# Kernel tuning notes

Hardware: AMD Instinct MI355X
Metric: run time of the kernel (lower is better)

Reference implementation:

```python
import jax, jax.numpy as jnp
import numpy as np

EPS = 1e-6
QMAX = 127.0


def _smooth_quant_linear(x, w):
    """SmoothQuant int8 linear: out = dequant(quant(x/s) @ quant(w*s)^T).
    x: [T, D] activations, w: [O, D] weights. Returns [T, O] float32.
    """
    amax_x = jnp.max(jnp.abs(x), axis=0)          # [D] per-in-channel act max
    amax_w = jnp.max(jnp.abs(w), axis=0)          # [D] per-in-channel weight max
    # smooth scale s_j = sqrt(amax_x_j / amax_w_j)  (alpha = 0.5)
    s = jnp.sqrt(jnp.maximum(amax_x, EPS) / jnp.maximum(amax_w, EPS))
    s = jnp.maximum(s, EPS)
    xs = x / s                                    # smoothed activations
    ws = w * s                                    # smoothed weights
    x_scale = jnp.maximum(jnp.max(jnp.abs(xs), axis=-1, keepdims=True), EPS) / QMAX  # [T,1] per-token
    w_scale = jnp.maximum(jnp.max(jnp.abs(ws), axis=-1, keepdims=True), EPS) / QMAX  # [O,1] per-row
    x_q = jnp.clip(jnp.round(xs / x_scale), -QMAX, QMAX)   # int8-valued, kept f32 for GEMM
    w_q = jnp.clip(jnp.round(ws / w_scale), -QMAX, QMAX)
    # int8 GEMM + dequant with per-token / per-channel scales
    return (x_q @ w_q.T) * x_scale * w_scale.T


def _expert_forward(xe, guw, dw):
    # xe: [T, dim], guw: [2*ims, dim], dw: [dim, ims]
    h = _smooth_quant_linear(xe, guw)             # [T, 2*ims]
    gate, up = jnp.split(h, 2, axis=-1)           # [T, ims] each
    a = jax.nn.silu(gate) * up                    # SwiGLU
    return _smooth_quant_linear(a, dw)            # [T, dim]


def setup_inputs() -> dict:
    key = jax.random.key(0)
    k1, k2, k3 = jax.random.split(key, 3)
    E, T, D, I = 8, 2048, 2048, 1024
    x = jax.random.normal(k1, (E, T, D), dtype=jnp.float32)
    gate_up_weight = jax.random.normal(k2, (E, 2 * I, D), dtype=jnp.float32) * 0.02
    down_weight = jax.random.normal(k3, (E, D, I), dtype=jnp.float32) * 0.02
    return {"x": x, "gate_up_weight": gate_up_weight, "down_weight": down_weight}


def reference(x, gate_up_weight, down_weight):
    # Grouped per-expert SmoothQuant SwiGLU MLP: vmap over the expert axis.
    return jax.vmap(_expert_forward)(x, gate_up_weight, down_weight)
```

## Files before the change

kernel.cpp:

```cpp
#include <hip/hip_runtime.h>
#include <stdint.h>

constexpr int E_ = 8, T_ = 2048, D_ = 2048, I_ = 1024;
#define EPS_ 1e-6f
#define QMAX_ 127.0f

typedef int v4i __attribute__((ext_vector_type(4)));
typedef uint32_t __attribute__((address_space(1))) u32g_t;
typedef uint32_t __attribute__((address_space(3))) u32l_t;

__device__ __forceinline__ void load_lds16(const void* g, void* l) {
  __builtin_amdgcn_global_load_lds((u32g_t*)(uintptr_t)g, (u32l_t*)(uintptr_t)l,
                                   16, 0, 0);
}

template <int RPC>
__global__ __launch_bounds__(256) void colmax_partial(
    const float* __restrict__ src, float* __restrict__ partial, int cols) {
  int e = blockIdx.z, rc = blockIdx.y;
  int col = blockIdx.x * 256 + threadIdx.x;
  const float* p = src + ((size_t)e * gridDim.y + rc) * RPC * cols + col;
  float m = 0.f;
#pragma unroll 8
  for (int r = 0; r < RPC; ++r) m = fmaxf(m, fabsf(p[(size_t)r * cols]));
  partial[((size_t)e * gridDim.y + rc) * cols + col] = m;
}

__global__ __launch_bounds__(256) void compute_s(
    const float* __restrict__ px, const float* __restrict__ pw,
    float* __restrict__ s, int cols) {
  int e = blockIdx.y;
  int c = blockIdx.x * 256 + threadIdx.x;
  float ax = 0.f, aw = 0.f;
  for (int k = 0; k < 16; ++k) {
    ax = fmaxf(ax, px[((size_t)e * 16 + k) * cols + c]);
    aw = fmaxf(aw, pw[((size_t)e * 16 + k) * cols + c]);
  }
  float sv = sqrtf(fmaxf(ax, EPS_) / fmaxf(aw, EPS_));
  s[(size_t)e * cols + c] = fmaxf(sv, EPS_);
}

template <bool MUL, int COLS>
__global__ __launch_bounds__(256) void quant_rows(
    const float* __restrict__ src, const float* __restrict__ s,
    int8_t* __restrict__ q, float* __restrict__ rscale, int nrows) {
  constexpr int NP = COLS / 256;
  int e = blockIdx.y;
  int row = blockIdx.x * 4 + (threadIdx.x >> 6);
  int lane = threadIdx.x & 63;
  const float4* row4 = (const float4*)(src + ((size_t)e * nrows + row) * COLS);
  const float4* s4 = (const float4*)(s + (size_t)e * COLS);
  float4 vv[NP];
  float m = 0.f;
#pragma unroll
  for (int i = 0; i < NP; ++i) {
    int c = i * 64 + lane;
    float4 rv = row4[c], sv = s4[c];
    float4 v;
    v.x = MUL ? rv.x * sv.x : rv.x / sv.x;
    v.y = MUL ? rv.y * sv.y : rv.y / sv.y;
    v.z = MUL ? rv.z * sv.z : rv.z / sv.z;
    v.w = MUL ? rv.w * sv.w : rv.w / sv.w;
    vv[i] = v;
    m = fmaxf(m, fmaxf(fmaxf(fabsf(v.x), fabsf(v.y)), fmaxf(fabsf(v.z), fabsf(v.w))));
  }
#pragma unroll
  for (int off = 32; off > 0; off >>= 1) m = fmaxf(m, __shfl_xor(m, off, 64));
  float scale = fmaxf(m, EPS_) / QMAX_;
  char4* qrow = (char4*)(q + ((size_t)e * nrows + row) * COLS);
#pragma unroll
  for (int i = 0; i < NP; ++i) {
    int c = i * 64 + lane;
    float4 v = vv[i];
    char4 o;
    o.x = (int8_t)fminf(fmaxf(rintf(v.x / scale), -QMAX_), QMAX_);
    o.y = (int8_t)fminf(fmaxf(rintf(v.y / scale), -QMAX_), QMAX_);
    o.z = (int8_t)fminf(fmaxf(rintf(v.z / scale), -QMAX_), QMAX_);
    o.w = (int8_t)fminf(fmaxf(rintf(v.w / scale), -QMAX_), QMAX_);
    qrow[c] = o;
  }
  if (lane == 0) rscale[(size_t)e * nrows + row] = scale;
}

template <bool FUSE, int K, int NOUT>
__global__ __launch_bounds__(256) void gemm_i8(
    const int8_t* __restrict__ Aq, const int8_t* __restrict__ Bq,
    const float* __restrict__ asc, const float* __restrict__ bsc,
    float* __restrict__ outp, float* __restrict__ pmax) {
  constexpr int BK = 64;
  constexpr int NK = K / BK;
  constexpr int NCH = FUSE ? 16 : 12;
  constexpr int CPW = NCH / 4;
  constexpr int TOT = 8192 + (FUSE ? 8192 : 4096);
  __shared__ int8_t lds[2][TOT];

  const int e = blockIdx.z;
  const int n0 = blockIdx.x * 64, m0 = blockIdx.y * 128;
  const int8_t* Ae = Aq + (size_t)e * T_ * K;
  const int8_t* Be = Bq + (size_t)e * 2048 * K;
  const int tid = threadIdx.x;
  const int lane = tid & 63, wv = tid >> 6;
  const int l16 = lane & 15, quad = lane >> 4;
  const int wm = wv & 1, wn = wv >> 1;
  const int lrow = lane >> 2;
  const int scol = ((lane & 3) ^ ((lane >> 3) & 3)) << 4;
  const int swsel = ((quad ^ ((l16 >> 1) & 3)) << 4);

  const int8_t* gsrc[CPW];
  int loff[CPW];
#pragma unroll
  for (int i = 0; i < CPW; ++i) {
    int c = wv * CPW + i;
    if (c < 8) {
      gsrc[i] = Ae + (size_t)(m0 + c * 16 + lrow) * K + scol;
      loff[i] = c * 1024;
    } else {
      int cc = c - 8;
      int br = n0 + ((FUSE && cc >= 4) ? I_ : 0) + (cc & 3) * 16 + lrow;
      gsrc[i] = Be + (size_t)br * K + scol;
      loff[i] = 8192 + cc * 1024;
    }
  }

  v4i accg[4][2], accu[4][2];
#pragma unroll
  for (int mt = 0; mt < 4; ++mt)
#pragma unroll
    for (int nt = 0; nt < 2; ++nt) {
      accg[mt][nt] = (v4i){0, 0, 0, 0};
      accu[mt][nt] = (v4i){0, 0, 0, 0};
    }

#pragma unroll
  for (int i = 0; i < CPW; ++i) load_lds16(gsrc[i], &lds[0][loff[i]]);
  __syncthreads();

  int cur = 0;
  for (int ks = 0; ks < NK; ++ks) {
    if (ks + 1 < NK) {
#pragma unroll
      for (int i = 0; i < CPW; ++i)
        load_lds16(gsrc[i] + (size_t)(ks + 1) * BK, &lds[cur ^ 1][loff[i]]);
    }
    const int8_t* La = &lds[cur][0];
    const int8_t* Lb = &lds[cur][8192];
    v4i af[4];
#pragma unroll
    for (int mt = 0; mt < 4; ++mt)
      af[mt] = *(const v4i*)(La + (wm * 64 + mt * 16 + l16) * 64 + swsel);
    v4i bf0[2], bf1[2];
#pragma unroll
    for (int nt = 0; nt < 2; ++nt) {
      int br = wn * 32 + nt * 16 + l16;
      bf0[nt] = *(const v4i*)(Lb + br * 64 + swsel);
      if (FUSE) bf1[nt] = *(const v4i*)(Lb + 4096 + br * 64 + swsel);
    }
#pragma unroll
    for (int mt = 0; mt < 4; ++mt)
#pragma unroll
      for (int nt = 0; nt < 2; ++nt) {
        accg[mt][nt] = __builtin_amdgcn_mfma_i32_16x16x64_i8(
            af[mt], bf0[nt], accg[mt][nt], 0, 0, 0);
        if (FUSE)
          accu[mt][nt] = __builtin_amdgcn_mfma_i32_16x16x64_i8(
              af[mt], bf1[nt], accu[mt][nt], 0, 0, 0);
      }
    __syncthreads();
    cur ^= 1;
  }

  const float* ascE = asc + (size_t)e * T_;
  const float* bscE = bsc + (size_t)e * 2048;
  float cml[2] = {0.f, 0.f};
#pragma unroll
  for (int mt = 0; mt < 4; ++mt)
#pragma unroll
    for (int nt = 0; nt < 2; ++nt)
#pragma unroll
      for (int r2 = 0; r2 < 4; ++r2) {
        int grow = m0 + wm * 64 + mt * 16 + quad * 4 + r2;
        int gcol = n0 + wn * 32 + nt * 16 + l16;
        float as = ascE[grow];
        if (FUSE) {
          float g = (float)accg[mt][nt][r2] * as * bscE[gcol];
          float u = (float)accu[mt][nt][r2] * as * bscE[I_ + gcol];
          float sg = g / (1.0f + expf(-g));
          float av = sg * u;
          outp[(size_t)e * T_ * NOUT + (size_t)grow * NOUT + gcol] = av;
          cml[nt] = fmaxf(cml[nt], fabsf(av));
        } else {
          outp[(size_t)e * T_ * NOUT + (size_t)grow * NOUT + gcol] =
              (float)accg[mt][nt][r2] * as * bscE[gcol];
        }
      }

  if (FUSE) {
    float* cmax = (float*)&lds[0][0];
    if (tid < 64) cmax[tid] = 0.f;
    __syncthreads();
#pragma unroll
    for (int nt = 0; nt < 2; ++nt)
      atomicMax((int*)&cmax[wn * 32 + nt * 16 + l16], __float_as_int(cml[nt]));
    __syncthreads();
    if (tid < 64)
      pmax[((size_t)e * 16 + blockIdx.y) * NOUT + n0 + tid] = cmax[tid];
  }
}

extern "C" void kernel_launch(void* const* d_in, const int* in_sizes, int n_in,
                              void* d_out, int out_size, void* d_ws, size_t ws_size,
                              hipStream_t stream) {
  const float* x   = (const float*)d_in[0];
  const float* guw = (const float*)d_in[1];
  const float* dw  = (const float*)d_in[2];
  float* out = (float*)d_out;

  char* ws = (char*)d_ws;
  size_t off = 0;
  auto alloc = [&](size_t bytes) { char* p = ws + off; off += bytes; return p; };
  int8_t* xq   = (int8_t*)alloc((size_t)E_ * T_ * D_);
  int8_t* wq1  = (int8_t*)alloc((size_t)E_ * 2 * I_ * D_);
  int8_t* aq   = (int8_t*)alloc((size_t)E_ * T_ * I_);
  int8_t* dwq  = (int8_t*)alloc((size_t)E_ * D_ * I_);
  float*  a    = (float*)alloc((size_t)E_ * T_ * I_ * 4);
  float*  px   = (float*)alloc((size_t)E_ * 16 * D_ * 4);
  float*  pw   = (float*)alloc((size_t)E_ * 16 * D_ * 4);
  float*  pdw  = (float*)alloc((size_t)E_ * 16 * I_ * 4);
  float*  pa   = (float*)alloc((size_t)E_ * 16 * I_ * 4);
  float*  s1   = (float*)alloc((size_t)E_ * D_ * 4);
  float*  s2   = (float*)alloc((size_t)E_ * I_ * 4);
  float*  xsc  = (float*)alloc((size_t)E_ * T_ * 4);
  float*  wsc1 = (float*)alloc((size_t)E_ * 2 * I_ * 4);
  float*  asc  = (float*)alloc((size_t)E_ * T_ * 4);
  float*  dwsc = (float*)alloc((size_t)E_ * D_ * 4);

  dim3 b(256);
  colmax_partial<128><<<dim3(D_ / 256, 16, E_), b, 0, stream>>>(x, px, D_);
  colmax_partial<128><<<dim3(D_ / 256, 16, E_), b, 0, stream>>>(guw, pw, D_);
  colmax_partial<128><<<dim3(I_ / 256, 16, E_), b, 0, stream>>>(dw, pdw, I_);
  compute_s<<<dim3(D_ / 256, E_), b, 0, stream>>>(px, pw, s1, D_);
  quant_rows<false, D_><<<dim3(T_ / 4, E_), b, 0, stream>>>(x, s1, xq, xsc, T_);
  quant_rows<true, D_><<<dim3(2 * I_ / 4, E_), b, 0, stream>>>(guw, s1, wq1, wsc1, 2 * I_);
  gemm_i8<true, D_, I_><<<dim3(I_ / 64, T_ / 128, E_), b, 0, stream>>>(
      xq, wq1, xsc, wsc1, a, pa);
  compute_s<<<dim3(I_ / 256, E_), b, 0, stream>>>(pa, pdw, s2, I_);
  quant_rows<false, I_><<<dim3(T_ / 4, E_), b, 0, stream>>>(a, s2, aq, asc, T_);
  quant_rows<true, I_><<<dim3(D_ / 4, E_), b, 0, stream>>>(dw, s2, dwq, dwsc, D_);
  gemm_i8<false, I_, D_><<<dim3(D_ / 64, T_ / 128, E_), b, 0, stream>>>(
      aq, dwq, asc, dwsc, out, nullptr);
}
```

Baseline: 601.0 us.

## Deepen GEMM pipeline to 4-slot LDS ring, widen down-proj tile, merge small launches

The int8 GEMM moves from a double buffer to a 4-slot LDS ring that prefetches two K-steps ahead. It uses explicit vmcnt waits and raw barriers instead of __syncthreads, and raises wave priority around the MFMA block. The down-projection GEMM now uses a 128-wide N tile so each block does more work per A load. The column-max kernels for x and gate/up are merged into one launch, and each activation/weight quantisation pair is merged into one launch to cut launch overhead. The larger LDS footprint (64KB per block) may reduce occupancy, and the hardcoded vmcnt literals tie correctness to exactly 4 chunks per wave.

```diff
diff --git a/kernel.cpp b/kernel.cpp
--- a/kernel.cpp
+++ b/kernel.cpp
@@ -12,6 +12,23 @@
 __device__ __forceinline__ void load_lds16(const void* g, void* l) {
   __builtin_amdgcn_global_load_lds((u32g_t*)(uintptr_t)g, (u32l_t*)(uintptr_t)l,
                                    16, 0, 0);
+}
+
+__global__ __launch_bounds__(256) void colmax_xw(
+    const float* __restrict__ x, const float* __restrict__ guw,
+    float* __restrict__ px, float* __restrict__ pw) {
+  int e = blockIdx.z, rc = blockIdx.y;
+  const float* src;
+  float* dst;
+  int rcc;
+  if (rc < 16) { src = x;   dst = px; rcc = rc; }
+  else         { src = guw; dst = pw; rcc = rc - 16; }
+  int col = blockIdx.x * 256 + threadIdx.x;
+  const float* p = src + ((size_t)e * 16 + rcc) * 128 * 2048 + col;
+  float m = 0.f;
+#pragma unroll 8
+  for (int r = 0; r < 128; ++r) m = fmaxf(m, fabsf(p[(size_t)r * 2048]));
+  dst[((size_t)e * 16 + rcc) * 2048 + col] = m;
 }
 
 template <int RPC>
@@ -41,15 +58,10 @@
 }
 
 template <bool MUL, int COLS>
-__global__ __launch_bounds__(256) void quant_rows(
-    const float* __restrict__ src, const float* __restrict__ s,
-    int8_t* __restrict__ q, float* __restrict__ rscale, int nrows) {
+__device__ __forceinline__ void quant_row_body(
+    const float4* __restrict__ row4, const float4* __restrict__ s4,
+    char4* __restrict__ qrow, float* __restrict__ rsc, int lane) {
   constexpr int NP = COLS / 256;
-  int e = blockIdx.y;
-  int row = blockIdx.x * 4 + (threadIdx.x >> 6);
-  int lane = threadIdx.x & 63;
-  const float4* row4 = (const float4*)(src + ((size_t)e * nrows + row) * COLS);
-  const float4* s4 = (const float4*)(s + (size_t)e * COLS);
   float4 vv[NP];
   float m = 0.f;
 #pragma unroll
@@ -67,7 +79,6 @@
 #pragma unroll
   for (int off = 32; off > 0; off >>= 1) m = fmaxf(m, __shfl_xor(m, off, 64));
   float scale = fmaxf(m, EPS_) / QMAX_;
-  char4* qrow = (char4*)(q + ((size_t)e * nrows + row) * COLS);
 #pragma unroll
   for (int i = 0; i < NP; ++i) {
     int c = i * 64 + lane;
@@ -79,23 +90,50 @@
     o.w = (int8_t)fminf(fmaxf(rintf(v.w / scale), -QMAX_), QMAX_);
     qrow[c] = o;
   }
-  if (lane == 0) rscale[(size_t)e * nrows + row] = scale;
-}
-
-template <bool FUSE, int K, int NOUT>
+  if (lane == 0) *rsc = scale;
+}
+
+template <int COLS>
+__global__ __launch_bounds__(256) void quant_pair(
+    const float* __restrict__ srcA, const float* __restrict__ srcB,
+    const float* __restrict__ s, int8_t* __restrict__ qA,
+    int8_t* __restrict__ qB, float* __restrict__ rscA,
+    float* __restrict__ rscB, int nrowsA, int nrowsB) {
+  int e = blockIdx.y;
+  int nbA = nrowsA >> 2;
+  bool isB = (int)blockIdx.x >= nbA;
+  int rb = isB ? (int)blockIdx.x - nbA : (int)blockIdx.x;
+  int row = rb * 4 + (threadIdx.x >> 6);
+  int lane = threadIdx.x & 63;
+  const float4* s4 = (const float4*)(s + (size_t)e * COLS);
+  if (isB) {
+    const float4* row4 = (const float4*)(srcB + ((size_t)e * nrowsB + row) * COLS);
+    char4* qrow = (char4*)(qB + ((size_t)e * nrowsB + row) * COLS);
+    quant_row_body<true, COLS>(row4, s4, qrow, rscB + (size_t)e * nrowsB + row, lane);
+  } else {
+    const float4* row4 = (const float4*)(srcA + ((size_t)e * nrowsA + row) * COLS);
+    char4* qrow = (char4*)(qA + ((size_t)e * nrowsA + row) * COLS);
+    quant_row_body<false, COLS>(row4, s4, qrow, rscA + (size_t)e * nrowsA + row, lane);
+  }
+}
+
+template <bool FUSE, int K, int NOUT, int BN>
 __global__ __launch_bounds__(256) void gemm_i8(
     const int8_t* __restrict__ Aq, const int8_t* __restrict__ Bq,
     const float* __restrict__ asc, const float* __restrict__ bsc,
     float* __restrict__ outp, float* __restrict__ pmax) {
-  constexpr int BK = 64;
+  constexpr int BM = 128, BK = 64;
   constexpr int NK = K / BK;
-  constexpr int NCH = FUSE ? 16 : 12;
+  constexpr int NBT = FUSE ? 2 : 1;
+  constexpr int SLOT = BM * 64 + NBT * BN * 64;
+  constexpr int NCH = SLOT / 1024;
   constexpr int CPW = NCH / 4;
-  constexpr int TOT = 8192 + (FUSE ? 8192 : 4096);
-  __shared__ int8_t lds[2][TOT];
+  constexpr int NT = BN / 32;
+  static_assert(CPW == 4, "vmcnt literals assume 4 chunks/wave");
+  __shared__ int8_t lds[4][SLOT];
 
   const int e = blockIdx.z;
-  const int n0 = blockIdx.x * 64, m0 = blockIdx.y * 128;
+  const int n0 = blockIdx.x * BN, m0 = blockIdx.y * BM;
   const int8_t* Ae = Aq + (size_t)e * T_ * K;
   const int8_t* Be = Bq + (size_t)e * 2048 * K;
   const int tid = threadIdx.x;
@@ -116,70 +154,82 @@
       loff[i] = c * 1024;
     } else {
       int cc = c - 8;
-      int br = n0 + ((FUSE && cc >= 4) ? I_ : 0) + (cc & 3) * 16 + lrow;
+      int br;
+      if (FUSE) br = n0 + (cc >= 4 ? I_ : 0) + (cc & 3) * 16 + lrow;
+      else      br = n0 + cc * 16 + lrow;
       gsrc[i] = Be + (size_t)br * K + scol;
       loff[i] = 8192 + cc * 1024;
     }
   }
 
-  v4i accg[4][2], accu[4][2];
+  v4i accg[4][NT], accu[4][NT];
 #pragma unroll
   for (int mt = 0; mt < 4; ++mt)
 #pragma unroll
-    for (int nt = 0; nt < 2; ++nt) {
+    for (int nt = 0; nt < NT; ++nt) {
       accg[mt][nt] = (v4i){0, 0, 0, 0};
       accu[mt][nt] = (v4i){0, 0, 0, 0};
     }
 
-#pragma unroll
-  for (int i = 0; i < CPW; ++i) load_lds16(gsrc[i], &lds[0][loff[i]]);
-  __syncthreads();
-
-  int cur = 0;
+  auto issue = [&](int ksrc, int slot) {
+#pragma unroll
+    for (int i = 0; i < CPW; ++i)
+      load_lds16(gsrc[i] + (size_t)ksrc * BK, &lds[slot][loff[i]]);
+  };
+
+  issue(0, 0);
+  issue(1, 1);
+
   for (int ks = 0; ks < NK; ++ks) {
-    if (ks + 1 < NK) {
-#pragma unroll
-      for (int i = 0; i < CPW; ++i)
-        load_lds16(gsrc[i] + (size_t)(ks + 1) * BK, &lds[cur ^ 1][loff[i]]);
-    }
-    const int8_t* La = &lds[cur][0];
-    const int8_t* Lb = &lds[cur][8192];
+    const int sl = ks & 3;
+    if (ks + 2 < NK) issue(ks + 2, (ks + 2) & 3);
+    const int rem = NK - 1 - ks;
+    if (rem >= 2)      asm volatile("s_waitcnt vmcnt(8)" ::: "memory");
+    else if (rem == 1) asm volatile("s_waitcnt vmcnt(4)" ::: "memory");
+    else               asm volatile("s_waitcnt vmcnt(0)" ::: "memory");
+    __builtin_amdgcn_s_barrier();
+    __builtin_amdgcn_sched_barrier(0);
+
+    const int8_t* La = &lds[sl][0];
+    const int8_t* Lb = &lds[sl][8192];
     v4i af[4];
 #pragma unroll
     for (int mt = 0; mt < 4; ++mt)
       af[mt] = *(const v4i*)(La + (wm * 64 + mt * 16 + l16) * 64 + swsel);
-    v4i bf0[2], bf1[2];
-#pragma unroll
-    for (int nt = 0; nt < 2; ++nt) {
-      int br = wn * 32 + nt * 16 + l16;
+    v4i bf0[NT], bf1[NT];
+#pragma unroll
+    for (int nt = 0; nt < NT; ++nt) {
+      int br = wn * (BN / 2) + nt * 16 + l16;
       bf0[nt] = *(const v4i*)(Lb + br * 64 + swsel);
       if (FUSE) bf1[nt] = *(const v4i*)(Lb + 4096 + br * 64 + swsel);
     }
+    __builtin_amdgcn_s_setprio(1);
 #pragma unroll
     for (int mt = 0; mt < 4; ++mt)
 #pragma unroll
-      for (int nt = 0; nt < 2; ++nt) {
+      for (int nt = 0; nt < NT; ++nt) {
         accg[mt][nt] = __builtin_amdgcn_mfma_i32_16x16x64_i8(
             af[mt], bf0[nt], accg[mt][nt], 0, 0, 0);
         if (FUSE)
           accu[mt][nt] = __builtin_amdgcn_mfma_i32_16x16x64_i8(
               af[mt], bf1[nt], accu[mt][nt], 0, 0, 0);
       }
-    __syncthreads();
-    cur ^= 1;
+    __builtin_amdgcn_s_setprio(0);
   }
 
   const float* ascE = asc + (size_t)e * T_;
   const float* bscE = bsc + (size_t)e * 2048;
-  float cml[2] = {0.f, 0.f};
+  float cml[NT];
+#pragma unroll
+  for (int nt = 0; nt < NT; ++nt) cml[nt] = 0.f;
 #pragma unroll
   for (int mt = 0; mt < 4; ++mt)
 #pragma unroll
-    for (int nt = 0; nt < 2; ++nt)
+    for (int nt = 0; nt < NT; ++nt)
 #pragma unroll
       for (int r2 = 0; r2 < 4; ++r2) {
         int grow = m0 + wm * 64 + mt * 16 + quad * 4 + r2;
-        int gcol = n0 + wn * 32 + nt * 16 + l16;
+        int gcol = n0 + wn * (BN / 2) + nt * 16 + l16;
         float as = ascE[grow];
         if (FUSE) {
           float g = (float)accg[mt][nt][r2] * as * bscE[gcol];
@@ -196,13 +246,14 @@
 
   if (FUSE) {
     float* cmax = (float*)&lds[0][0];
-    if (tid < 64) cmax[tid] = 0.f;
+    if (tid < BN) cmax[tid] = 0.f;
     __syncthreads();
 #pragma unroll
-    for (int nt = 0; nt < 2; ++nt)
-      atomicMax((int*)&cmax[wn * 32 + nt * 16 + l16], __float_as_int(cml[nt]));
+    for (int nt = 0; nt < NT; ++nt)
+      atomicMax((int*)&cmax[wn * (BN / 2) + nt * 16 + l16],
+                __float_as_int(cml[nt]));
     __syncthreads();
-    if (tid < 64)
+    if (tid < BN)
       pmax[((size_t)e * 16 + blockIdx.y) * NOUT + n0 + tid] = cmax[tid];
   }
 }
@@ -235,17 +286,16 @@
   float*  dwsc = (float*)alloc((size_t)E_ * D_ * 4);
 
   dim3 b(256);
-  colmax_partial<128><<<dim3(D_ / 256, 16, E_), b, 0, stream>>>(x, px, D_);
-  colmax_partial<128><<<dim3(D_ / 256, 16, E_), b, 0, stream>>>(guw, pw, D_);
+  colmax_xw<<<dim3(D_ / 256, 32, E_), b, 0, stream>>>(x, guw, px, pw);
   colmax_partial<128><<<dim3(I_ / 256, 16, E_), b, 0, stream>>>(dw, pdw, I_);
   compute_s<<<dim3(D_ / 256, E_), b, 0, stream>>>(px, pw, s1, D_);
-  quant_rows<false, D_><<<dim3(T_ / 4, E_), b, 0, stream>>>(x, s1, xq, xsc, T_);
-  quant_rows<true, D_><<<dim3(2 * I_ / 4, E_), b, 0, stream>>>(guw, s1, wq1, wsc1, 2 * I_);
-  gemm_i8<true, D_, I_><<<dim3(I_ / 64, T_ / 128, E_), b, 0, stream>>>(
+  quant_pair<D_><<<dim3((T_ + 2 * I_) / 4, E_), b, 0, stream>>>(
+      x, guw, s1, xq, wq1, xsc, wsc1, T_, 2 * I_);
+  gemm_i8<true, D_, I_, 64><<<dim3(I_ / 64, T_ / 128, E_), b, 0, stream>>>(
       xq, wq1, xsc, wsc1, a, pa);
   compute_s<<<dim3(I_ / 256, E_), b, 0, stream>>>(pa, pdw, s2, I_);
-  quant_rows<false, I_><<<dim3(T_ / 4, E_), b, 0, stream>>>(a, s2, aq, asc, T_);
-  quant_rows<true, I_><<<dim3(D_ / 4, E_), b, 0, stream>>>(dw, s2, dwq, dwsc, D_);
-  gemm_i8<false, I_, D_><<<dim3(D_ / 64, T_ / 128, E_), b, 0, stream>>>(
+  quant_pair<I_><<<dim3((T_ + D_) / 4, E_), b, 0, stream>>>(
+      a, dw, s2, aq, dwq, asc, dwsc, T_, D_);
+  gemm_i8<false, I_, D_, 128><<<dim3(D_ / 128, T_ / 128, E_), b, 0, stream>>>(
       aq, dwq, asc, dwsc, out, nullptr);
 }
```

Result: slower. 630.0 us (+4.8%).
